# Kernel optimization log

Measured on AMD Instinct MI355X. Metric: run time of the kernel, lower is better.

## Reference

```python
import jax, jax.numpy as jnp
import numpy as np

N_NODES = 10000
N_EDGES = 640000
IN, HID, OUT = 128, 256, 128


def setup_inputs() -> dict:
    key = jax.random.key(0)
    ks = jax.random.split(key, 8)
    scale_in = 1.0 / np.sqrt(IN)
    scale_hid = 1.0 / np.sqrt(HID)
    return {
        "x": jax.random.normal(ks[0], (N_NODES, IN), dtype=jnp.float32),
        "w_self1": jax.random.normal(ks[1], (IN, HID), dtype=jnp.float32) * scale_in,
        "w_neigh1": jax.random.normal(ks[2], (IN, HID), dtype=jnp.float32) * scale_in,
        "b1": jnp.zeros((HID,), dtype=jnp.float32),
        "w_self2": jax.random.normal(ks[3], (HID, OUT), dtype=jnp.float32) * scale_hid,
        "w_neigh2": jax.random.normal(ks[4], (HID, OUT), dtype=jnp.float32) * scale_hid,
        "b2": jnp.zeros((OUT,), dtype=jnp.float32),
        "src": jax.random.randint(ks[5], (N_EDGES,), 0, N_NODES, dtype=jnp.int64 if jax.config.jax_enable_x64 else jnp.int32),
        "dst": jax.random.randint(ks[6], (N_EDGES,), 0, N_NODES, dtype=jnp.int64 if jax.config.jax_enable_x64 else jnp.int32),
    }


def _mean_agg(h, src, dst, n_nodes):
    # gather source features along edges, segment-sum into destinations, divide by in-degree
    summed = jax.ops.segment_sum(h[src], dst, num_segments=n_nodes)  # [N, d]
    deg = jax.ops.segment_sum(jnp.ones_like(dst, dtype=h.dtype), dst, num_segments=n_nodes)
    return summed / jnp.maximum(deg, 1.0)[:, None]


def _sage_layer(h, src, dst, w_self, w_neigh, b):
    neigh = _mean_agg(h, src, dst, h.shape[0])
    return h @ w_self + neigh @ w_neigh + b


def reference(x, w_self1, w_neigh1, b1, w_self2, w_neigh2, b2, src, dst):
    h = _sage_layer(x, src, dst, w_self1, w_neigh1, b1)
    h = jax.nn.relu(h)  # dropout = identity in eval mode
    h = _sage_layer(h, src, dst, w_self2, w_neigh2, b2)
    return h
```

## Files before the change

### kernel.cpp

```cpp
#include <hip/hip_runtime.h>

#define N_NODES 10000
#define N_EDGES 640000
#define DIM_IN  128
#define DIM_HID 256
#define DIM_OUT 128
#define NPAD    10240
#define NBUCK   80
#define NPB     128
#define NBLKA   160
#define EPB     4000

typedef __attribute__((ext_vector_type(8))) short bf16x8;
typedef __attribute__((ext_vector_type(4))) float f32x4;

__device__ __forceinline__ unsigned short f2bf(float f) {
    unsigned int u = __float_as_uint(f);
    return (unsigned short)((u + 0x7fffu + ((u >> 16) & 1u)) >> 16);
}
__device__ __forceinline__ float bf2f(unsigned short h) {
    return __uint_as_float(((unsigned int)h) << 16);
}
__device__ __forceinline__ float bflo(unsigned int u) { return __uint_as_float(u << 16); }
__device__ __forceinline__ float bfhi(unsigned int u) { return __uint_as_float(u & 0xffff0000u); }

__global__ __launch_bounds__(256)
void countA_kernel(const int* __restrict__ dst, int* __restrict__ cntAT) {
    __shared__ int c[NBUCK];
    const int tid = threadIdx.x, blk = blockIdx.x;
    if (tid < NBUCK) c[tid] = 0;
    __syncthreads();
    const int e0 = blk * EPB;
    for (int i = tid; i < EPB; i += 256) atomicAdd(&c[dst[e0 + i] >> 7], 1);
    __syncthreads();
    if (tid < NBUCK) cntAT[tid * NBLKA + blk] = c[tid];
}

__global__ __launch_bounds__(64)
void scanB_kernel(const int* __restrict__ cntAT, int* __restrict__ runoffT) {
    const int lane = threadIdx.x;
    const int base = lane * (NBUCK * NBLKA / 64);
    int s = 0;
    for (int i = 0; i < NBUCK * NBLKA / 64; ++i) s += cntAT[base + i];
    int incl = s;
#pragma unroll
    for (int d = 1; d < 64; d <<= 1) {
        int u = __shfl_up(incl, d);
        if (lane >= d) incl += u;
    }
    int run = incl - s;
    for (int i = 0; i < NBUCK * NBLKA / 64; ++i) {
        runoffT[base + i] = run;
        run += cntAT[base + i];
    }
}

__global__ __launch_bounds__(256)
void scatterA_kernel(const int* __restrict__ src, const int* __restrict__ dst,
                     const int* __restrict__ runoffT,
                     int* __restrict__ srcb, int* __restrict__ dstb) {
    __shared__ int cur[NBUCK];
    const int tid = threadIdx.x, blk = blockIdx.x;
    if (tid < NBUCK) cur[tid] = runoffT[tid * NBLKA + blk];
    __syncthreads();
    const int e0 = blk * EPB;
    for (int i = tid; i < EPB; i += 256) {
        int s = src[e0 + i], d = dst[e0 + i];
        int pos = atomicAdd(&cur[d >> 7], 1);
        srcb[pos] = s;
        dstb[pos] = d;
    }
}

__global__ __launch_bounds__(256)
void binB_kernel(const int* __restrict__ srcb, const int* __restrict__ dstb,
                 const int* __restrict__ runoffT, int* __restrict__ off,
                 float* __restrict__ invdeg, int* __restrict__ sorted_src) {
    __shared__ int cnt[NPB];
    __shared__ int curs[NPB];
    const int tid = threadIdx.x, b = blockIdx.x;
    const int base = runoffT[b * NBLKA];
    const int end  = (b == NBUCK - 1) ? N_EDGES : runoffT[(b + 1) * NBLKA];
    if (tid < NPB) cnt[tid] = 0;
    __syncthreads();
    for (int e = base + tid; e < end; e += 256) atomicAdd(&cnt[dstb[e] & (NPB - 1)], 1);
    __syncthreads();
    if (tid < 64) {
        int c0 = cnt[tid * 2], c1 = cnt[tid * 2 + 1];
        int s = c0 + c1;
        int incl = s;
#pragma unroll
        for (int d = 1; d < 64; d <<= 1) {
            int u = __shfl_up(incl, d);
            if (tid >= d) incl += u;
        }
        int run = incl - s;
        curs[tid * 2] = run;
        curs[tid * 2 + 1] = run + c0;
    }
    __syncthreads();
    if (tid < NPB) {
        int n = b * NPB + tid;
        off[n] = base + curs[tid];
        if (n < N_NODES) invdeg[n] = 1.0f / fmaxf((float)cnt[tid], 1.0f);
        if (n == NPAD - 1) off[NPAD] = N_EDGES;
    }
    __syncthreads();
    for (int e = base + tid; e < end; e += 256) {
        int n = dstb[e] & (NPB - 1);
        int pos = base + atomicAdd(&curs[n], 1);
        sorted_src[pos] = srcb[e];
    }
}

__global__ __launch_bounds__(256)
void prep_kernel(const float* __restrict__ x, unsigned short* __restrict__ xb,
                 const float* __restrict__ w1s, const float* __restrict__ w1n,
                 const float* __restrict__ w2s, const float* __restrict__ w2n,
                 unsigned short* __restrict__ o1s, unsigned short* __restrict__ o1n,
                 unsigned short* __restrict__ o2s, unsigned short* __restrict__ o2n) {
    const int tid = threadIdx.x, blk = blockIdx.x;
    if (blk < 1250) {
        int i = blk * 256 + tid;
        float4 v = ((const float4*)x)[i];
        ushort4 o;
        o.x = f2bf(v.x); o.y = f2bf(v.y); o.z = f2bf(v.z); o.w = f2bf(v.w);
        ((ushort4*)xb)[i] = o;
    } else {
        int which = (blk - 1250) >> 7;
        const float* w = (which == 0) ? w1s : (which == 1) ? w1n : (which == 2) ? w2s : w2n;
        unsigned short* o = (which == 0) ? o1s : (which == 1) ? o1n : (which == 2) ? o2s : o2n;
        int K = (which < 2) ? DIM_IN : DIM_HID;
        int N = (which < 2) ? DIM_HID : DIM_OUT;
        int idx = ((blk - 1250) & 127) * 256 + tid;
        int n = idx / K, k = idx - n * K;
        o[n * K + k] = f2bf(w[k * N + n]);
    }
}

__global__ __launch_bounds__(64)
void agg_kernel(const unsigned short* __restrict__ feat, const int* __restrict__ sorted_src,
                const int* __restrict__ off, const float* __restrict__ invdeg,
                unsigned short* __restrict__ outa) {
    const int n = blockIdx.x;
    const int lane = threadIdx.x;
    const int s0 = off[n], s1 = off[n + 1];
    __shared__ int sidx[64];
    float a0 = 0.f, b0 = 0.f, a1 = 0.f, b1 = 0.f;
    float a2 = 0.f, b2 = 0.f, a3 = 0.f, b3 = 0.f;
    for (int base = s0; base < s1; base += 64) {
        sidx[lane] = sorted_src[min(base + lane, s1 - 1)];
        __syncthreads();
        int c = min(64, s1 - base);
        int i = 0;
        for (; i + 4 <= c; i += 4) {
            unsigned int u0 = *(const unsigned int*)&feat[(size_t)sidx[i + 0] * 128 + 2 * lane];
            unsigned int u1 = *(const unsigned int*)&feat[(size_t)sidx[i + 1] * 128 + 2 * lane];
            unsigned int u2 = *(const unsigned int*)&feat[(size_t)sidx[i + 2] * 128 + 2 * lane];
            unsigned int u3 = *(const unsigned int*)&feat[(size_t)sidx[i + 3] * 128 + 2 * lane];
            a0 += bflo(u0); b0 += bfhi(u0);
            a1 += bflo(u1); b1 += bfhi(u1);
            a2 += bflo(u2); b2 += bfhi(u2);
            a3 += bflo(u3); b3 += bfhi(u3);
        }
        for (; i < c; ++i) {
            unsigned int u = *(const unsigned int*)&feat[(size_t)sidx[i] * 128 + 2 * lane];
            a0 += bflo(u); b0 += bfhi(u);
        }
        __syncthreads();
    }
    float inv = invdeg[n];
    float slo = ((a0 + a1) + (a2 + a3)) * inv;
    float shi = ((b0 + b1) + (b2 + b3)) * inv;
    unsigned int packed = (unsigned int)f2bf(slo) | ((unsigned int)f2bf(shi) << 16);
    *(unsigned int*)&outa[(size_t)n * 128 + 2 * lane] = packed;
}

template<int PASSES, bool RELU, bool HAS_EPI, bool OUT_BF16>
__launch_bounds__(256)
__global__ void mfma_gemm(const unsigned short* __restrict__ A1, const unsigned short* __restrict__ B1T,
                          const unsigned short* __restrict__ A2, const unsigned short* __restrict__ B2T,
                          const unsigned short* __restrict__ epi, const float* __restrict__ bias,
                          void* __restrict__ Cout, int M, int N, int K) {
    const int tid = threadIdx.x;
    const int w = tid >> 6, lane = tid & 63;
    const int m0 = blockIdx.x * 64, n0 = blockIdx.y * 64;
    const int l15 = lane & 15;
    const int koff = (lane >> 4) * 8;
    const int rowc = min(m0 + w * 16 + l15, M - 1);

    f32x4 acc[4] = {};
#pragma unroll
    for (int pass = 0; pass < PASSES; ++pass) {
        const unsigned short* __restrict__ A  = (PASSES == 2 && pass) ? A2 : A1;
        const unsigned short* __restrict__ BT = (PASSES == 2 && pass) ? B2T : B1T;
        const unsigned short* arow = A + (size_t)rowc * K;
        for (int k0 = 0; k0 < K; k0 += 32) {
            bf16x8 af = *(const bf16x8*)(arow + k0 + koff);
#pragma unroll
            for (int f = 0; f < 4; ++f) {
                const unsigned short* brow = BT + (size_t)(n0 + f * 16 + l15) * K;
                bf16x8 bfr = *(const bf16x8*)(brow + k0 + koff);
                acc[f] = __builtin_amdgcn_mfma_f32_16x16x32_bf16(af, bfr, acc[f], 0, 0, 0);
            }
        }
    }

#pragma unroll
    for (int f = 0; f < 4; ++f) {
        int col = n0 + f * 16 + l15;
        float bv = bias ? bias[col] : 0.f;
#pragma unroll
        for (int r = 0; r < 4; ++r) {
            int grow = m0 + w * 16 + (lane >> 4) * 4 + r;
            if (grow < M) {
                float v = acc[f][r] + bv;
                if (HAS_EPI) v += bf2f(epi[(size_t)grow * N + col]);
                if (RELU) v = fmaxf(v, 0.f);
                if (OUT_BF16) ((unsigned short*)Cout)[(size_t)grow * N + col] = f2bf(v);
                else          ((float*)Cout)[(size_t)grow * N + col] = v;
            }
        }
    }
}

extern "C" void kernel_launch(void* const* d_in, const int* in_sizes, int n_in,
                              void* d_out, int out_size, void* d_ws, size_t ws_size,
                              hipStream_t stream) {
    const float* x        = (const float*)d_in[0];
    const float* w_self1  = (const float*)d_in[1];
    const float* w_neigh1 = (const float*)d_in[2];
    const float* b1       = (const float*)d_in[3];
    const float* w_self2  = (const float*)d_in[4];
    const float* w_neigh2 = (const float*)d_in[5];
    const float* b2       = (const float*)d_in[6];
    const int*   src      = (const int*)d_in[7];
    const int*   dst      = (const int*)d_in[8];
    float* out = (float*)d_out;

    char* p = (char*)d_ws;
    auto alloc = [&](size_t bytes) { char* q = p; p += (bytes + 1023) & ~(size_t)1023; return q; };
    int*            cntAT      = (int*)alloc(NBUCK * NBLKA * 4);
    int*            runoffT    = (int*)alloc(NBUCK * NBLKA * 4);
    int*            srcb       = (int*)alloc((size_t)N_EDGES * 4);
    int*            dstb       = (int*)alloc((size_t)N_EDGES * 4);
    int*            off        = (int*)alloc((NPAD + 1) * 4);
    int*            sorted_src = (int*)alloc((size_t)N_EDGES * 4);
    float*          invdeg     = (float*)alloc(NPAD * 4);
    unsigned short* xb         = (unsigned short*)alloc((size_t)N_NODES * DIM_IN * 2);
    unsigned short* w1sT       = (unsigned short*)alloc(DIM_IN * DIM_HID * 2);
    unsigned short* w1nT       = (unsigned short*)alloc(DIM_IN * DIM_HID * 2);
    unsigned short* w2sT       = (unsigned short*)alloc(DIM_HID * DIM_OUT * 2);
    unsigned short* w2nT       = (unsigned short*)alloc(DIM_HID * DIM_OUT * 2);
    unsigned short* aggbuf     = (unsigned short*)alloc((size_t)N_NODES * 128 * 2);
    unsigned short* h          = (unsigned short*)alloc((size_t)N_NODES * DIM_HID * 2);
    unsigned short* t          = (unsigned short*)alloc((size_t)N_NODES * DIM_OUT * 2);

    countA_kernel  <<<NBLKA, 256, 0, stream>>>(dst, cntAT);
    scanB_kernel   <<<1, 64, 0, stream>>>(cntAT, runoffT);
    scatterA_kernel<<<NBLKA, 256, 0, stream>>>(src, dst, runoffT, srcb, dstb);
    binB_kernel    <<<NBUCK, 256, 0, stream>>>(srcb, dstb, runoffT, off, invdeg, sorted_src);

    prep_kernel<<<1250 + 512, 256, 0, stream>>>(x, xb, w_self1, w_neigh1, w_self2, w_neigh2,
                                                w1sT, w1nT, w2sT, w2nT);

    agg_kernel<<<N_NODES, 64, 0, stream>>>(xb, sorted_src, off, invdeg, aggbuf);
    mfma_gemm<2, true, false, true><<<dim3(157, DIM_HID / 64), 256, 0, stream>>>(
        xb, w1sT, aggbuf, w1nT, nullptr, b1, h, N_NODES, DIM_HID, DIM_IN);

    mfma_gemm<1, false, false, true><<<dim3(157, DIM_OUT / 64), 256, 0, stream>>>(
        h, w2nT, nullptr, nullptr, nullptr, nullptr, t, N_NODES, DIM_OUT, DIM_HID);
    agg_kernel<<<N_NODES, 64, 0, stream>>>(t, sorted_src, off, invdeg, aggbuf);
    mfma_gemm<1, false, true, false><<<dim3(157, DIM_OUT / 64), 256, 0, stream>>>(
        h, w2sT, nullptr, nullptr, aggbuf, b2, out, N_NODES, DIM_OUT, DIM_HID);
}
```

Baseline: 204.8 us.

## Fuse layer-2 self/neigh GEMMs and fold aggregation into final output

Layer 2 previously ran separate GEMMs for the neighbour and self weights, reading h twice, then a separate aggregation and an epilogue GEMM. Now one kernel computes both products from a single read of h, writing t in bf16 and the self part in fp32 to a new buffer. The aggregation kernel then adds the bias and the self part directly into the output. This removes one GEMM launch, one h read and the aggbuf round trip, at the cost of writing and reading an extra fp32 intermediate.

Result: faster. 194.3 us (-5.1%).

```diff
diff --git a/kernel.cpp b/kernel.cpp
--- a/kernel.cpp
+++ b/kernel.cpp
@@ -176,11 +176,11 @@
     *(unsigned int*)&outa[(size_t)n * 128 + 2 * lane] = packed;
 }
 
-template<int PASSES, bool RELU, bool HAS_EPI, bool OUT_BF16>
+template<int PASSES, bool RELU, bool OUT_BF16>
 __launch_bounds__(256)
 __global__ void mfma_gemm(const unsigned short* __restrict__ A1, const unsigned short* __restrict__ B1T,
                           const unsigned short* __restrict__ A2, const unsigned short* __restrict__ B2T,
-                          const unsigned short* __restrict__ epi, const float* __restrict__ bias,
+                          const float* __restrict__ bias,
                           void* __restrict__ Cout, int M, int N, int K) {
     const int tid = threadIdx.x;
     const int w = tid >> 6, lane = tid & 63;
@@ -215,13 +215,97 @@
             int grow = m0 + w * 16 + (lane >> 4) * 4 + r;
             if (grow < M) {
                 float v = acc[f][r] + bv;
-                if (HAS_EPI) v += bf2f(epi[(size_t)grow * N + col]);
                 if (RELU) v = fmaxf(v, 0.f);
                 if (OUT_BF16) ((unsigned short*)Cout)[(size_t)grow * N + col] = f2bf(v);
                 else          ((float*)Cout)[(size_t)grow * N + col] = v;
             }
         }
     }
+}
+
+__launch_bounds__(256)
+__global__ void gemm23_kernel(const unsigned short* __restrict__ A,
+                              const unsigned short* __restrict__ BnT,
+                              const unsigned short* __restrict__ BsT,
+                              unsigned short* __restrict__ t, float* __restrict__ outbase,
+                              int M, int N, int K) {
+    const int tid = threadIdx.x;
+    const int w = tid >> 6, lane = tid & 63;
+    const int m0 = blockIdx.x * 64, n0 = blockIdx.y * 64;
+    const int l15 = lane & 15;
+    const int koff = (lane >> 4) * 8;
+    const int rowc = min(m0 + w * 16 + l15, M - 1);
+
+    f32x4 accn[4] = {};
+    f32x4 accs[4] = {};
+    const unsigned short* arow = A + (size_t)rowc * K;
+    for (int k0 = 0; k0 < K; k0 += 32) {
+        bf16x8 af = *(const bf16x8*)(arow + k0 + koff);
+#pragma unroll
+        for (int f = 0; f < 4; ++f) {
+            const unsigned short* bnrow = BnT + (size_t)(n0 + f * 16 + l15) * K;
+            const unsigned short* bsrow = BsT + (size_t)(n0 + f * 16 + l15) * K;
+            bf16x8 bn = *(const bf16x8*)(bnrow + k0 + koff);
+            bf16x8 bs = *(const bf16x8*)(bsrow + k0 + koff);
+            accn[f] = __builtin_amdgcn_mfma_f32_16x16x32_bf16(af, bn, accn[f], 0, 0, 0);
+            accs[f] = __builtin_amdgcn_mfma_f32_16x16x32_bf16(af, bs, accs[f], 0, 0, 0);
+        }
+    }
+
+#pragma unroll
+    for (int f = 0; f < 4; ++f) {
+        int col = n0 + f * 16 + l15;
+#pragma unroll
+        for (int r = 0; r < 4; ++r) {
+            int grow = m0 + w * 16 + (lane >> 4) * 4 + r;
+            if (grow < M) {
+                t[(size_t)grow * N + col]       = f2bf(accn[f][r]);
+                outbase[(size_t)grow * N + col] = accs[f][r];
+            }
+        }
+    }
+}
+
+__global__ __launch_bounds__(64)
+void aggadd_kernel(const unsigned short* __restrict__ t, const int* __restrict__ sorted_src,
+                   const int* __restrict__ off, const float* __restrict__ invdeg,
+                   const float* __restrict__ outbase, const float* __restrict__ bias,
+                   float* __restrict__ out) {
+    const int n = blockIdx.x;
+    const int lane = threadIdx.x;
+    const int s0 = off[n], s1 = off[n + 1];
+    __shared__ int sidx[64];
+    float a0 = 0.f, b0 = 0.f, a1 = 0.f, b1 = 0.f;
+    float a2 = 0.f, b2v = 0.f, a3 = 0.f, b3 = 0.f;
+    for (int base = s0; base < s1; base += 64) {
+        sidx[lane] = sorted_src[min(base + lane, s1 - 1)];
+        __syncthreads();
+        int c = min(64, s1 - base);
+        int i = 0;
+        for (; i + 4 <= c; i += 4) {
+            unsigned int u0 = *(const unsigned int*)&t[(size_t)sidx[i + 0] * 128 + 2 * lane];
+            unsigned int u1 = *(const unsigned int*)&t[(size_t)sidx[i + 1] * 128 + 2 * lane];
+            unsigned int u2 = *(const unsigned int*)&t[(size_t)sidx[i + 2] * 128 + 2 * lane];
+            unsigned int u3 = *(const unsigned int*)&t[(size_t)sidx[i + 3] * 128 + 2 * lane];
+            a0 += bflo(u0); b0 += bfhi(u0);
+            a1 += bflo(u1); b1 += bfhi(u1);
+            a2 += bflo(u2); b2v += bfhi(u2);
+            a3 += bflo(u3); b3 += bfhi(u3);
+        }
+        for (; i < c; ++i) {
+            unsigned int u = *(const unsigned int*)&t[(size_t)sidx[i] * 128 + 2 * lane];
+            a0 += bflo(u); b0 += bfhi(u);
+        }
+        __syncthreads();
+    }
+    float inv = invdeg[n];
+    float slo = ((a0 + a1) + (a2 + a3)) * inv;
+    float shi = ((b0 + b1) + (b2v + b3)) * inv;
+    float2 ob = *(const float2*)&outbase[(size_t)n * 128 + 2 * lane];
+    float2 o;
+    o.x = (ob.x + bias[2 * lane])     + slo;
+    o.y = (ob.y + bias[2 * lane + 1]) + shi;
+    *(float2*)&out[(size_t)n * 128 + 2 * lane] = o;
 }
 
 extern "C" void kernel_launch(void* const* d_in, const int* in_sizes, int n_in,
@@ -255,6 +339,7 @@
     unsigned short* aggbuf     = (unsigned short*)alloc((size_t)N_NODES * 128 * 2);
     unsigned short* h          = (unsigned short*)alloc((size_t)N_NODES * DIM_HID * 2);
     unsigned short* t          = (unsigned short*)alloc((size_t)N_NODES * DIM_OUT * 2);
+    float*          outbase    = (float*)alloc((size_t)N_NODES * DIM_OUT * 4);
 
     countA_kernel  <<<NBLKA, 256, 0, stream>>>(dst, cntAT);
     scanB_kernel   <<<1, 64, 0, stream>>>(cntAT, runoffT);
@@ -265,12 +350,10 @@
                                                 w1sT, w1nT, w2sT, w2nT);
 
     agg_kernel<<<N_NODES, 64, 0, stream>>>(xb, sorted_src, off, invdeg, aggbuf);
-    mfma_gemm<2, true, false, true><<<dim3(157, DIM_HID / 64), 256, 0, stream>>>(
-        xb, w1sT, aggbuf, w1nT, nullptr, b1, h, N_NODES, DIM_HID, DIM_IN);
-
-    mfma_gemm<1, false, false, true><<<dim3(157, DIM_OUT / 64), 256, 0, stream>>>(
-        h, w2nT, nullptr, nullptr, nullptr, nullptr, t, N_NODES, DIM_OUT, DIM_HID);
-    agg_kernel<<<N_NODES, 64, 0, stream>>>(t, sorted_src, off, invdeg, aggbuf);
-    mfma_gemm<1, false, true, false><<<dim3(157, DIM_OUT / 64), 256, 0, stream>>>(
-        h, w2sT, nullptr, nullptr, aggbuf, b2, out, N_NODES, DIM_OUT, DIM_HID);
-}
+    mfma_gemm<2, true, true><<<dim3(157, DIM_HID / 64), 256, 0, stream>>>(
+        xb, w1sT, aggbuf, w1nT, b1, h, N_NODES, DIM_HID, DIM_IN);
+
+    gemm23_kernel<<<dim3(157, DIM_OUT / 64), 256, 0, stream>>>(
+        h, w2nT, w2sT, t, outbase, N_NODES, DIM_OUT, DIM_HID);
+    aggadd_kernel<<<N_NODES, 64, 0, stream>>>(t, sorted_src, off, invdeg, outbase, b2, out);
+}
```
